# Optimization experiments

Measured on AMD Instinct MI355X. Metric: run time of the kernel, lower is better.

## Reference

```python
import jax, jax.numpy as jnp
import numpy as np

# Standard bitsandbytes NF4 codebook (16 values)
NF4_CODE = jnp.array([
    -1.0, -0.6961928009986877, -0.5250730514526367, -0.39491748809814453,
    -0.28444138169288635, -0.18477343022823334, -0.09105003625154495, 0.0,
    0.07958029955625534, 0.16093020141124725, 0.24611230194568634,
    0.33791524171829224, 0.44070982933044434, 0.5626170039176941,
    0.7229568362236023, 1.0], dtype=jnp.float32)

BLOCKSIZE = 64
IN_FEATURES = 4096
OUT_FEATURES = 11008


def setup_inputs() -> dict:
    key = jax.random.key(0)
    k1, k2, k3, k4 = jax.random.split(key, 4)
    x = jax.random.normal(k1, (4, 2048, IN_FEATURES), dtype=jnp.float32)
    weight_q = jax.random.randint(k2, (OUT_FEATURES, IN_FEATURES), 0, 16, dtype=jnp.int32)
    absmax = jax.random.uniform(k3, (OUT_FEATURES, IN_FEATURES // BLOCKSIZE), dtype=jnp.float32)
    bias = jax.random.normal(k4, (OUT_FEATURES,), dtype=jnp.float32)
    return {"x": x, "weight_q": weight_q, "absmax": absmax, "bias": bias}


def reference(x, weight_q, absmax, bias):
    out_f, in_f = weight_q.shape
    # Blockwise NF4 dequantization: code lookup * per-block absmax scale
    w_code = NF4_CODE[weight_q]                                   # [O, I]
    w_blocks = w_code.reshape(out_f, in_f // BLOCKSIZE, BLOCKSIZE)
    w = (w_blocks * absmax[:, :, None]).reshape(out_f, in_f)      # [O, I]
    # Linear: y = x @ W^T + b
    y = jnp.einsum('bsi,oi->bso', x, w) + bias
    return y
```

## Files before the change

### kernel.cpp

```cpp
#include <hip/hip_runtime.h>
#include <hip/hip_bf16.h>
#include <stdint.h>

typedef __attribute__((ext_vector_type(8))) short short8;
typedef __attribute__((ext_vector_type(8))) unsigned short ushort8;
typedef __attribute__((ext_vector_type(4))) float f32x4;

#define K_DIM 4096
#define N_DIM 11008
#define M_DIM 8192
#define BM 256
#define BN 256
#define BK 32
#define TILES (K_DIM / BK)

__constant__ float c_nf4[16] = {
    -1.0f, -0.6961928009986877f, -0.5250730514526367f, -0.39491748809814453f,
    -0.28444138169288635f, -0.18477343022823334f, -0.09105003625154495f, 0.0f,
    0.07958029955625534f, 0.16093020141124725f, 0.24611230194568634f,
    0.33791524171829224f, 0.44070982933044434f, 0.5626170039176941f,
    0.7229568362236023f, 1.0f};

__device__ __forceinline__ unsigned short f2bf(float f) {
    uint32_t u = __float_as_uint(f);
    u += 0x7fffu + ((u >> 16) & 1u);
    return (unsigned short)(u >> 16);
}

__global__ __launch_bounds__(256) void nf4_dequant_w(const int* __restrict__ q,
                                                     const float* __restrict__ absmax,
                                                     unsigned short* __restrict__ w) {
    __shared__ float lut[16];
    if (threadIdx.x < 16) lut[threadIdx.x] = c_nf4[threadIdx.x];
    __syncthreads();
    size_t t = (size_t)blockIdx.x * 256 + threadIdx.x;
    const int4* q4 = (const int4*)q;
    int4 qa = q4[2 * t];
    int4 qb = q4[2 * t + 1];
    float s = absmax[t >> 3];
    ushort8 o;
    o[0] = f2bf(lut[qa.x & 15] * s);
    o[1] = f2bf(lut[qa.y & 15] * s);
    o[2] = f2bf(lut[qa.z & 15] * s);
    o[3] = f2bf(lut[qa.w & 15] * s);
    o[4] = f2bf(lut[qb.x & 15] * s);
    o[5] = f2bf(lut[qb.y & 15] * s);
    o[6] = f2bf(lut[qb.z & 15] * s);
    o[7] = f2bf(lut[qb.w & 15] * s);
    ((ushort8*)w)[t] = o;
}

__global__ __launch_bounds__(256) void x_to_bf16(const float* __restrict__ x,
                                                 unsigned short* __restrict__ xb) {
    size_t t = (size_t)blockIdx.x * 256 + threadIdx.x;
    const float4* x4 = (const float4*)x;
    float4 a = x4[2 * t];
    float4 b = x4[2 * t + 1];
    ushort8 o;
    o[0] = f2bf(a.x); o[1] = f2bf(a.y); o[2] = f2bf(a.z); o[3] = f2bf(a.w);
    o[4] = f2bf(b.x); o[5] = f2bf(b.y); o[6] = f2bf(b.z); o[7] = f2bf(b.w);
    ((ushort8*)xb)[t] = o;
}

#define STAGE(gbase, region, j, k0)                                           \
  do {                                                                        \
    const int _row = (j) * 128 + (tid >> 2);                                  \
    const int _cp = tid & 3;                                                  \
    __builtin_amdgcn_global_load_lds(                                         \
        (const __attribute__((address_space(1))) void*)((gbase) +             \
            (size_t)_row * K_DIM + (k0) + _cp * 8),                           \
        (__attribute__((address_space(3))) void*)((region) +                  \
            ((j) * 512 + wave * 64) * 8),                                     \
        16, 0, 0);                                                            \
  } while (0)

#define MFMA4(mi_, Areg)                                                                  \
  acc[mi_][0] = __builtin_amdgcn_mfma_f32_16x16x32_bf16(Areg, b0, acc[mi_][0], 0, 0, 0);  \
  acc[mi_][1] = __builtin_amdgcn_mfma_f32_16x16x32_bf16(Areg, b1, acc[mi_][1], 0, 0, 0);  \
  acc[mi_][2] = __builtin_amdgcn_mfma_f32_16x16x32_bf16(Areg, b2, acc[mi_][2], 0, 0, 0);  \
  acc[mi_][3] = __builtin_amdgcn_mfma_f32_16x16x32_bf16(Areg, b3, acc[mi_][3], 0, 0, 0);

__global__ __launch_bounds__(512, 2) void gemm256(const unsigned short* __restrict__ A,
                                                  const unsigned short* __restrict__ B,
                                                  const float* __restrict__ bias,
                                                  float* __restrict__ C) {
    __shared__ unsigned short As[3][BM * BK];
    __shared__ unsigned short Bs[3][BN * BK];

    const int tid  = threadIdx.x;
    const int wave = tid >> 6;
    const int lane = tid & 63;
    const int wm = wave >> 2;
    const int wn = wave & 3;
    const int lr = lane & 15;
    const int lk = (lane >> 4) << 3;

    const int nbn = N_DIM / BN;
    const int cpx = (int)gridDim.x >> 3;
    const int bid = (int)blockIdx.x;
    const int swz = (bid & 7) * cpx + (bid >> 3);
    const int bm = swz / nbn;
    const int bn = swz % nbn;

    const unsigned short* Ab = A + (size_t)bm * BM * K_DIM;
    const unsigned short* Bb = B + (size_t)bn * BN * K_DIM;

    f32x4 acc[8][4];
#pragma unroll
    for (int i = 0; i < 8; ++i)
#pragma unroll
        for (int j = 0; j < 4; ++j)
#pragma unroll
            for (int v = 0; v < 4; ++v) acc[i][j][v] = 0.0f;

    STAGE(Ab, &As[0][0], 0, 0); STAGE(Bb, &Bs[0][0], 0, 0);
    STAGE(Ab, &As[0][0], 1, 0); STAGE(Bb, &Bs[0][0], 1, 0);
    STAGE(Ab, &As[1][0], 0, BK); STAGE(Bb, &Bs[1][0], 0, BK);
    STAGE(Ab, &As[1][0], 1, BK); STAGE(Bb, &Bs[1][0], 1, BK);
    asm volatile("s_waitcnt vmcnt(4)" ::: "memory");
    asm volatile("s_barrier" ::: "memory");

    int r = 0, r2 = 2;
#pragma unroll 1
    for (int t = 0; t < TILES; ++t) {
        int ts = t + 2; if (ts >= TILES) ts -= TILES;
        const int k0s = ts * BK;
        const unsigned short* Ar = &As[r][0];
        const unsigned short* Br = &Bs[r][0];
        unsigned short* Aw = &As[r2][0];
        unsigned short* Bw = &Bs[r2][0];

        short8 a0 = *(const short8*)(Ar + (wm * 128 +  0 + lr) * BK + lk);
        short8 a1 = *(const short8*)(Ar + (wm * 128 + 16 + lr) * BK + lk);
        short8 a2 = *(const short8*)(Ar + (wm * 128 + 32 + lr) * BK + lk);
        short8 a3 = *(const short8*)(Ar + (wm * 128 + 48 + lr) * BK + lk);
        short8 b0 = *(const short8*)(Br + (wn * 64 +  0 + lr) * BK + lk);
        short8 b1 = *(const short8*)(Br + (wn * 64 + 16 + lr) * BK + lk);
        short8 b2 = *(const short8*)(Br + (wn * 64 + 32 + lr) * BK + lk);
        short8 b3 = *(const short8*)(Br + (wn * 64 + 48 + lr) * BK + lk);
        STAGE(Ab, Aw, 0, k0s);
        STAGE(Bb, Bw, 0, k0s);
        asm volatile("s_barrier" ::: "memory");
        asm volatile("s_waitcnt lgkmcnt(0)" ::: "memory");
        __builtin_amdgcn_sched_barrier(0);
        __builtin_amdgcn_s_setprio(1);
        MFMA4(0, a0) MFMA4(1, a1) MFMA4(2, a2) MFMA4(3, a3)
        __builtin_amdgcn_s_setprio(0);
        __builtin_amdgcn_sched_barrier(0);
        asm volatile("s_barrier" ::: "memory");

        a0 = *(const short8*)(Ar + (wm * 128 +  64 + lr) * BK + lk);
        a1 = *(const short8*)(Ar + (wm * 128 +  80 + lr) * BK + lk);
        a2 = *(const short8*)(Ar + (wm * 128 +  96 + lr) * BK + lk);
        a3 = *(const short8*)(Ar + (wm * 128 + 112 + lr) * BK + lk);
        STAGE(Ab, Aw, 1, k0s);
        STAGE(Bb, Bw, 1, k0s);
        asm volatile("s_barrier" ::: "memory");
        asm volatile("s_waitcnt lgkmcnt(0)" ::: "memory");
        __builtin_amdgcn_sched_barrier(0);
        __builtin_amdgcn_s_setprio(1);
        MFMA4(4, a0) MFMA4(5, a1) MFMA4(6, a2) MFMA4(7, a3)
        __builtin_amdgcn_s_setprio(0);
        __builtin_amdgcn_sched_barrier(0);
        asm volatile("s_waitcnt vmcnt(4)" ::: "memory");
        asm volatile("s_barrier" ::: "memory");

        r  = (r  == 2) ? 0 : r  + 1;
        r2 = (r2 == 2) ? 0 : r2 + 1;
    }
    asm volatile("s_waitcnt vmcnt(0)" ::: "memory");

    const int row0 = bm * BM + wm * 128 + ((lane >> 4) << 2);
    const int col0 = bn * BN + wn * 64 + lr;
#pragma unroll
    for (int ni = 0; ni < 4; ++ni) {
        const int col = col0 + ni * 16;
        const float bv = bias[col];
#pragma unroll
        for (int mi = 0; mi < 8; ++mi) {
#pragma unroll
            for (int v = 0; v < 4; ++v) {
                C[(size_t)(row0 + mi * 16 + v) * N_DIM + col] = acc[mi][ni][v] + bv;
            }
        }
    }
}

extern "C" void kernel_launch(void* const* d_in, const int* in_sizes, int n_in,
                              void* d_out, int out_size, void* d_ws, size_t ws_size,
                              hipStream_t stream) {
    const float* x    = (const float*)d_in[0];
    const int*   wq   = (const int*)d_in[1];
    const float* am   = (const float*)d_in[2];
    const float* bias = (const float*)d_in[3];
    float* out = (float*)d_out;

    const size_t w_elems = (size_t)N_DIM * K_DIM;
    const size_t x_elems = (size_t)M_DIM * K_DIM;
    const size_t need = (w_elems + x_elems) * sizeof(unsigned short);
    if (ws_size < need) return;

    unsigned short* wbf = (unsigned short*)d_ws;
    unsigned short* xbf = wbf + w_elems;

    nf4_dequant_w<<<(int)(w_elems / 8 / 256), 256, 0, stream>>>(wq, am, wbf);
    x_to_bf16<<<(int)(x_elems / 8 / 256), 256, 0, stream>>>(x, xbf);

    const int grid = (M_DIM / BM) * (N_DIM / BN);
    gemm256<<<grid, 512, 0, stream>>>(xbf, wbf, bias, out);
}
```

Measured before the change: 932.1 us.

## Add XOR-swizzled LDS layout and deepen GEMM prefetch to four buffers

The GEMM LDS staging now stores each 16-byte K-chunk at a slot XORed with the low two bits of its row, and the MFMA operand reads apply the same XOR. This is meant to spread the b128 LDS reads across banks and cut bank conflicts. The shared-memory ring grows from three to four stages with three tiles prefetched ahead, and the vmcnt wait thresholds are adjusted to match, to hide more global-load latency. The cost is more LDS per block (now 128KB), which still allows only one block per CU.

```diff
diff --git a/kernel.cpp b/kernel.cpp
--- a/kernel.cpp
+++ b/kernel.cpp
@@ -13,6 +13,7 @@
 #define BN 256
 #define BK 32
 #define TILES (K_DIM / BK)
+#define NBUF 4
 
 __constant__ float c_nf4[16] = {
     -1.0f, -0.6961928009986877f, -0.5250730514526367f, -0.39491748809814453f,
@@ -66,9 +67,10 @@
   do {                                                                        \
     const int _row = (j) * 128 + (tid >> 2);                                  \
     const int _cp = tid & 3;                                                  \
+    const int _col = ((_cp ^ (_row & 3)) << 3);                               \
     __builtin_amdgcn_global_load_lds(                                         \
         (const __attribute__((address_space(1))) void*)((gbase) +             \
-            (size_t)_row * K_DIM + (k0) + _cp * 8),                           \
+            (size_t)_row * K_DIM + (k0) + _col),                              \
         (__attribute__((address_space(3))) void*)((region) +                  \
             ((j) * 512 + wave * 64) * 8),                                     \
         16, 0, 0);                                                            \
@@ -84,8 +86,8 @@
                                                   const unsigned short* __restrict__ B,
                                                   const float* __restrict__ bias,
                                                   float* __restrict__ C) {
-    __shared__ unsigned short As[3][BM * BK];
-    __shared__ unsigned short Bs[3][BN * BK];
+    __shared__ unsigned short As[NBUF][BM * BK];
+    __shared__ unsigned short Bs[NBUF][BN * BK];
 
     const int tid  = threadIdx.x;
     const int wave = tid >> 6;
@@ -94,6 +96,7 @@
     const int wn = wave & 3;
     const int lr = lane & 15;
     const int lk = (lane >> 4) << 3;
+    const int sw = lk ^ ((lr & 3) << 3);
 
     const int nbn = N_DIM / BN;
     const int cpx = (int)gridDim.x >> 3;
@@ -113,31 +116,33 @@
 #pragma unroll
             for (int v = 0; v < 4; ++v) acc[i][j][v] = 0.0f;
 
-    STAGE(Ab, &As[0][0], 0, 0); STAGE(Bb, &Bs[0][0], 0, 0);
-    STAGE(Ab, &As[0][0], 1, 0); STAGE(Bb, &Bs[0][0], 1, 0);
-    STAGE(Ab, &As[1][0], 0, BK); STAGE(Bb, &Bs[1][0], 0, BK);
-    STAGE(Ab, &As[1][0], 1, BK); STAGE(Bb, &Bs[1][0], 1, BK);
-    asm volatile("s_waitcnt vmcnt(4)" ::: "memory");
+#pragma unroll
+    for (int p = 0; p < 3; ++p) {
+        STAGE(Ab, &As[p][0], 0, p * BK); STAGE(Bb, &Bs[p][0], 0, p * BK);
+        STAGE(Ab, &As[p][0], 1, p * BK); STAGE(Bb, &Bs[p][0], 1, p * BK);
+    }
+    asm volatile("s_waitcnt vmcnt(8)" ::: "memory");
     asm volatile("s_barrier" ::: "memory");
 
-    int r = 0, r2 = 2;
 #pragma unroll 1
     for (int t = 0; t < TILES; ++t) {
-        int ts = t + 2; if (ts >= TILES) ts -= TILES;
+        const int r  = t & (NBUF - 1);
+        const int rw = (t + 3) & (NBUF - 1);
+        int ts = t + 3; if (ts >= TILES) ts -= TILES;
         const int k0s = ts * BK;
         const unsigned short* Ar = &As[r][0];
         const unsigned short* Br = &Bs[r][0];
-        unsigned short* Aw = &As[r2][0];
-        unsigned short* Bw = &Bs[r2][0];
-
-        short8 a0 = *(const short8*)(Ar + (wm * 128 +  0 + lr) * BK + lk);
-        short8 a1 = *(const short8*)(Ar + (wm * 128 + 16 + lr) * BK + lk);
-        short8 a2 = *(const short8*)(Ar + (wm * 128 + 32 + lr) * BK + lk);
-        short8 a3 = *(const short8*)(Ar + (wm * 128 + 48 + lr) * BK + lk);
-        short8 b0 = *(const short8*)(Br + (wn * 64 +  0 + lr) * BK + lk);
-        short8 b1 = *(const short8*)(Br + (wn * 64 + 16 + lr) * BK + lk);
-        short8 b2 = *(const short8*)(Br + (wn * 64 + 32 + lr) * BK + lk);
-        short8 b3 = *(const short8*)(Br + (wn * 64 + 48 + lr) * BK + lk);
+        unsigned short* Aw = &As[rw][0];
+        unsigned short* Bw = &Bs[rw][0];
+
+        short8 a0 = *(const short8*)(Ar + (wm * 128 +  0 + lr) * BK + sw);
+        short8 a1 = *(const short8*)(Ar + (wm * 128 + 16 + lr) * BK + sw);
+        short8 a2 = *(const short8*)(Ar + (wm * 128 + 32 + lr) * BK + sw);
+        short8 a3 = *(const short8*)(Ar + (wm * 128 + 48 + lr) * BK + sw);
+        short8 b0 = *(const short8*)(Br + (wn * 64 +  0 + lr) * BK + sw);
+        short8 b1 = *(const short8*)(Br + (wn * 64 + 16 + lr) * BK + sw);
+        short8 b2 = *(const short8*)(Br + (wn * 64 + 32 + lr) * BK + sw);
+        short8 b3 = *(const short8*)(Br + (wn * 64 + 48 + lr) * BK + sw);
         STAGE(Ab, Aw, 0, k0s);
         STAGE(Bb, Bw, 0, k0s);
         asm volatile("s_barrier" ::: "memory");
@@ -149,10 +154,10 @@
         __builtin_amdgcn_sched_barrier(0);
         asm volatile("s_barrier" ::: "memory");
 
-        a0 = *(const short8*)(Ar + (wm * 128 +  64 + lr) * BK + lk);
-        a1 = *(const short8*)(Ar + (wm * 128 +  80 + lr) * BK + lk);
-        a2 = *(const short8*)(Ar + (wm * 128 +  96 + lr) * BK + lk);
-        a3 = *(const short8*)(Ar + (wm * 128 + 112 + lr) * BK + lk);
+        a0 = *(const short8*)(Ar + (wm * 128 +  64 + lr) * BK + sw);
+        a1 = *(const short8*)(Ar + (wm * 128 +  80 + lr) * BK + sw);
+        a2 = *(const short8*)(Ar + (wm * 128 +  96 + lr) * BK + sw);
+        a3 = *(const short8*)(Ar + (wm * 128 + 112 + lr) * BK + sw);
         STAGE(Ab, Aw, 1, k0s);
         STAGE(Bb, Bw, 1, k0s);
         asm volatile("s_barrier" ::: "memory");
@@ -162,11 +167,8 @@
         MFMA4(4, a0) MFMA4(5, a1) MFMA4(6, a2) MFMA4(7, a3)
         __builtin_amdgcn_s_setprio(0);
         __builtin_amdgcn_sched_barrier(0);
-        asm volatile("s_waitcnt vmcnt(4)" ::: "memory");
-        asm volatile("s_barrier" ::: "memory");
-
-        r  = (r  == 2) ? 0 : r  + 1;
-        r2 = (r2 == 2) ? 0 : r2 + 1;
+        asm volatile("s_waitcnt vmcnt(8)" ::: "memory");
+        asm volatile("s_barrier" ::: "memory");
     }
     asm volatile("s_waitcnt vmcnt(0)" ::: "memory");
 
```

Result: faster. 911.2 us (-2.2%).

## Double K tile to 64 with XOR-swizzled LDS and double-buffered split staging

Applied to the files above, without the earlier changes.

Raises BK from 32 to 64 and moves from a triple to a double LDS buffer. Each tile is staged in two row-halves so the waves whose data lives in the first half can start their LDS reads before the barrier. An XOR swizzle on the LDS layout is meant to avoid bank conflicts on the wider rows. Per-tile work becomes 64 MFMAs between barriers, halving the number of synchronisation points. The cost is a larger LDS footprint and a pipeline only one tile deep, which may expose more global-load latency.

```diff
diff --git a/kernel.cpp b/kernel.cpp
--- a/kernel.cpp
+++ b/kernel.cpp
@@ -11,7 +11,7 @@
 #define M_DIM 8192
 #define BM 256
 #define BN 256
-#define BK 32
+#define BK 64
 #define TILES (K_DIM / BK)
 
 __constant__ float c_nf4[16] = {
@@ -62,30 +62,49 @@
     ((ushort8*)xb)[t] = o;
 }
 
-#define STAGE(gbase, region, j, k0)                                           \
-  do {                                                                        \
-    const int _row = (j) * 128 + (tid >> 2);                                  \
-    const int _cp = tid & 3;                                                  \
-    __builtin_amdgcn_global_load_lds(                                         \
-        (const __attribute__((address_space(1))) void*)((gbase) +             \
-            (size_t)_row * K_DIM + (k0) + _cp * 8),                           \
-        (__attribute__((address_space(3))) void*)((region) +                  \
-            ((j) * 512 + wave * 64) * 8),                                     \
-        16, 0, 0);                                                            \
+#define STAGE_HALF(gbase, region, j, k0)                                    \
+  do {                                                                      \
+    _Pragma("unroll")                                                       \
+    for (int _g = 0; _g < 2; ++_g) {                                        \
+      const int _D = _g * 512 + tid;                \
+      const int _r = (j) * 128 + (_D >> 3);                                 \
+      const int _c = (_D & 7) ^ (_r & 7);                 \
+      __builtin_amdgcn_global_load_lds(                                     \
+          (const __attribute__((address_space(1))) void*)((gbase) +         \
+              (size_t)_r * K_DIM + (k0) + _c * 8),                          \
+          (__attribute__((address_space(3))) void*)((region) +              \
+              ((j) * 1024 + _g * 512 + wave * 64) * 8),                     \
+          16, 0, 0);                                                        \
+    }                                                                       \
   } while (0)
 
-#define MFMA4(mi_, Areg)                                                                  \
-  acc[mi_][0] = __builtin_amdgcn_mfma_f32_16x16x32_bf16(Areg, b0, acc[mi_][0], 0, 0, 0);  \
-  acc[mi_][1] = __builtin_amdgcn_mfma_f32_16x16x32_bf16(Areg, b1, acc[mi_][1], 0, 0, 0);  \
-  acc[mi_][2] = __builtin_amdgcn_mfma_f32_16x16x32_bf16(Areg, b2, acc[mi_][2], 0, 0, 0);  \
-  acc[mi_][3] = __builtin_amdgcn_mfma_f32_16x16x32_bf16(Areg, b3, acc[mi_][3], 0, 0, 0);
+#define READS(kksel)                                                        \
+  do {                                                                      \
+    _Pragma("unroll")                                                       \
+    for (int mi = 0; mi < 8; ++mi)                                          \
+      af[mi] = *(const short8*)(Ar + wm * 8192 + mi * 1024 + (roff ^ (kksel))); \
+    _Pragma("unroll")                                                       \
+    for (int ni = 0; ni < 4; ++ni)                                          \
+      bf[ni] = *(const short8*)(Br + wn * 4096 + ni * 1024 + (roff ^ (kksel))); \
+  } while (0)
+
+#define MFMA32                                                              \
+  do {                                                                      \
+    _Pragma("unroll")                                                       \
+    for (int mi = 0; mi < 8; ++mi) {                                        \
+      _Pragma("unroll")                                                     \
+      for (int ni = 0; ni < 4; ++ni)                                        \
+        acc[mi][ni] = __builtin_amdgcn_mfma_f32_16x16x32_bf16(              \
+            af[mi], bf[ni], acc[mi][ni], 0, 0, 0);                          \
+    }                                                                       \
+  } while (0)
 
 __global__ __launch_bounds__(512, 2) void gemm256(const unsigned short* __restrict__ A,
                                                   const unsigned short* __restrict__ B,
                                                   const float* __restrict__ bias,
                                                   float* __restrict__ C) {
-    __shared__ unsigned short As[3][BM * BK];
-    __shared__ unsigned short Bs[3][BN * BK];
+    __shared__ unsigned short As[2][BM * BK];
+    __shared__ unsigned short Bs[2][BN * BK];
 
     const int tid  = threadIdx.x;
     const int wave = tid >> 6;
@@ -93,7 +112,9 @@
     const int wm = wave >> 2;
     const int wn = wave & 3;
     const int lr = lane & 15;
-    const int lk = (lane >> 4) << 3;
+    const int q  = lane >> 4;
+    const int roff = lr * 64 + ((q ^ (lr & 7)) << 3);
+    const int early = (wave < 2);
 
     const int nbn = N_DIM / BN;
     const int cpx = (int)gridDim.x >> 3;
@@ -113,64 +134,44 @@
 #pragma unroll
             for (int v = 0; v < 4; ++v) acc[i][j][v] = 0.0f;
 
-    STAGE(Ab, &As[0][0], 0, 0); STAGE(Bb, &Bs[0][0], 0, 0);
-    STAGE(Ab, &As[0][0], 1, 0); STAGE(Bb, &Bs[0][0], 1, 0);
-    STAGE(Ab, &As[1][0], 0, BK); STAGE(Bb, &Bs[1][0], 0, BK);
-    STAGE(Ab, &As[1][0], 1, BK); STAGE(Bb, &Bs[1][0], 1, BK);
+    STAGE_HALF(Ab, &As[0][0], 0, 0); STAGE_HALF(Bb, &Bs[0][0], 0, 0);
+    STAGE_HALF(Ab, &As[0][0], 1, 0); STAGE_HALF(Bb, &Bs[0][0], 1, 0);
     asm volatile("s_waitcnt vmcnt(4)" ::: "memory");
     asm volatile("s_barrier" ::: "memory");
 
-    int r = 0, r2 = 2;
 #pragma unroll 1
     for (int t = 0; t < TILES; ++t) {
-        int ts = t + 2; if (ts >= TILES) ts -= TILES;
+        const int p = t & 1;
+        const unsigned short* Ar = &As[p][0];
+        const unsigned short* Br = &Bs[p][0];
+        unsigned short* Aw = &As[p ^ 1][0];
+        unsigned short* Bw = &Bs[p ^ 1][0];
+        int ts = t + 1; if (ts >= TILES) ts = 0;
         const int k0s = ts * BK;
-        const unsigned short* Ar = &As[r][0];
-        const unsigned short* Br = &Bs[r][0];
-        unsigned short* Aw = &As[r2][0];
-        unsigned short* Bw = &Bs[r2][0];
-
-        short8 a0 = *(const short8*)(Ar + (wm * 128 +  0 + lr) * BK + lk);
-        short8 a1 = *(const short8*)(Ar + (wm * 128 + 16 + lr) * BK + lk);
-        short8 a2 = *(const short8*)(Ar + (wm * 128 + 32 + lr) * BK + lk);
-        short8 a3 = *(const short8*)(Ar + (wm * 128 + 48 + lr) * BK + lk);
-        short8 b0 = *(const short8*)(Br + (wn * 64 +  0 + lr) * BK + lk);
-        short8 b1 = *(const short8*)(Br + (wn * 64 + 16 + lr) * BK + lk);
-        short8 b2 = *(const short8*)(Br + (wn * 64 + 32 + lr) * BK + lk);
-        short8 b3 = *(const short8*)(Br + (wn * 64 + 48 + lr) * BK + lk);
-        STAGE(Ab, Aw, 0, k0s);
-        STAGE(Bb, Bw, 0, k0s);
-        asm volatile("s_barrier" ::: "memory");
-        asm volatile("s_waitcnt lgkmcnt(0)" ::: "memory");
-        __builtin_amdgcn_sched_barrier(0);
-        __builtin_amdgcn_s_setprio(1);
-        MFMA4(0, a0) MFMA4(1, a1) MFMA4(2, a2) MFMA4(3, a3)
-        __builtin_amdgcn_s_setprio(0);
-        __builtin_amdgcn_sched_barrier(0);
-        asm volatile("s_barrier" ::: "memory");
-
-        a0 = *(const short8*)(Ar + (wm * 128 +  64 + lr) * BK + lk);
-        a1 = *(const short8*)(Ar + (wm * 128 +  80 + lr) * BK + lk);
-        a2 = *(const short8*)(Ar + (wm * 128 +  96 + lr) * BK + lk);
-        a3 = *(const short8*)(Ar + (wm * 128 + 112 + lr) * BK + lk);
-        STAGE(Ab, Aw, 1, k0s);
-        STAGE(Bb, Bw, 1, k0s);
-        asm volatile("s_barrier" ::: "memory");
-        asm volatile("s_waitcnt lgkmcnt(0)" ::: "memory");
-        __builtin_amdgcn_sched_barrier(0);
-        __builtin_amdgcn_s_setprio(1);
-        MFMA4(4, a0) MFMA4(5, a1) MFMA4(6, a2) MFMA4(7, a3)
-        __builtin_amdgcn_s_setprio(0);
-        __builtin_amdgcn_sched_barrier(0);
+
+        short8 af[8], bf[4];
+
+        STAGE_HALF(Ab, Aw, 0, k0s);
+        STAGE_HALF(Bb, Bw, 0, k0s);
+        if (early) READS(0);
         asm volatile("s_waitcnt vmcnt(4)" ::: "memory");
         asm volatile("s_barrier" ::: "memory");
-
-        r  = (r  == 2) ? 0 : r  + 1;
-        r2 = (r2 == 2) ? 0 : r2 + 1;
+        if (!early) READS(0);
+        STAGE_HALF(Ab, Aw, 1, k0s);
+        STAGE_HALF(Bb, Bw, 1, k0s);
+
+        __builtin_amdgcn_s_setprio(1);
+        MFMA32;
+        READS(32);
+        MFMA32;
+        __builtin_amdgcn_s_setprio(0);
+
+        asm volatile("s_waitcnt vmcnt(4)" ::: "memory");
+        asm volatile("s_barrier" ::: "memory");
     }
     asm volatile("s_waitcnt vmcnt(0)" ::: "memory");
 
-    const int row0 = bm * BM + wm * 128 + ((lane >> 4) << 2);
+    const int row0 = bm * BM + wm * 128 + (q << 2);
     const int col0 = bn * BN + wn * 64 + lr;
 #pragma unroll
     for (int ni = 0; ni < 4; ++ni) {
```

Result: slower. 992.3 us (+6.5%).
